# Kernel tuning notes

Measured on AMD Instinct MI355X. Metric: run time of the kernel, lower is better.

The kernel has to match this reference:

```python
import jax, jax.numpy as jnp
import numpy as np

EMBED_DIM = 1024
SCALE = float(np.sqrt(EMBED_DIM))


def setup_inputs() -> dict:
    key = jax.random.key(0)
    ks = jax.random.split(key, 4)
    B, S, D = 4, 2048, EMBED_DIM
    x = jax.random.normal(ks[0], (B, S, D), dtype=jnp.float32)
    # causal mask: 1 where attention allowed, 0 where blocked
    mask = jnp.tril(jnp.ones((S, S), dtype=jnp.int32))
    init = 1.0 / np.sqrt(D)
    Wq = jax.random.normal(ks[1], (D, D), dtype=jnp.float32) * init
    Wk = jax.random.normal(ks[2], (D, D), dtype=jnp.float32) * init
    Wv = jax.random.normal(ks[3], (D, D), dtype=jnp.float32) * init
    bq = jnp.zeros((D,), dtype=jnp.float32)
    bk = jnp.zeros((D,), dtype=jnp.float32)
    bv = jnp.zeros((D,), dtype=jnp.float32)
    return {"x": x, "mask": mask, "Wq": Wq, "bq": bq, "Wk": Wk, "bk": bk, "Wv": Wv, "bv": bv}


def reference(x, mask, Wq, bq, Wk, bk, Wv, bv):
    # Q, K, V projections (torch Linear: x @ W^T + b; here W stored as (D_in, D_out))
    q = x @ Wq + bq  # (B, S, D)
    k = x @ Wk + bk
    v = x @ Wv + bv
    # attention scores: Q K^T / sqrt(D)
    scores = jnp.einsum("bsd,btd->bst", q, k) / SCALE  # (B, S, S)
    scores = jnp.where(mask == 0, -jnp.inf, scores)
    attn = jax.nn.softmax(scores, axis=-1)
    # dropout disabled (inference / eval mode)
    out = jnp.einsum("bst,btd->bsd", attn, v)  # (B, S, D)
    return out
```

## Files before the change

### kernel.cpp

```cpp
#include <hip/hip_runtime.h>
#include <math.h>

#define DMODEL 1024
#define SEQ 2048
#define BATCH 4
#define SCALE_INV (1.0f/32.0f)

typedef unsigned short ushort_t;
typedef __attribute__((ext_vector_type(8))) short bf16x8;
typedef __attribute__((ext_vector_type(4))) float f32x4;

__device__ __forceinline__ ushort_t f2bf(float f) {
    unsigned int u = __float_as_uint(f);
    unsigned int rounding = 0x7FFFu + ((u >> 16) & 1u);
    return (ushort_t)((u + rounding) >> 16);
}

#define GLOAD16(SRC, DST) \
    __builtin_amdgcn_global_load_lds( \
        (const __attribute__((address_space(1))) void*)(SRC), \
        (__attribute__((address_space(3))) void*)(DST), 16, 0, 0)

__device__ __forceinline__ int xcd_swz(int bid, int nwg) {
    return (bid & 7) * (nwg >> 3) + (bid >> 3);
}

__device__ __forceinline__ void gemm_core_128(
    const ushort_t* __restrict__ A, int lda,
    const ushort_t* __restrict__ Bt, int ldb,
    int arow0, int brow0, int ksteps,
    ushort_t* As, ushort_t* Bs,
    f32x4 acc[4][4])
{
    const int tid = threadIdx.x;
    const int l   = tid & 63;
    const int w   = tid >> 6;
    const int wr  = w >> 1;
    const int wc  = w & 1;

    for (int s = 0; s < ksteps; ++s) {
        const int k0 = s * 32;
        #pragma unroll
        for (int i = 0; i < 2; ++i) {
            const int off = i * 4096 + w * 1024 + l * 16;
            const int row = off >> 6;
            const int ke  = (off & 63) >> 1;
            GLOAD16(A + (size_t)(arow0 + row) * lda + k0 + ke,
                    (char*)As + i * 4096 + w * 1024);
        }
        #pragma unroll
        for (int i = 0; i < 2; ++i) {
            const int off = i * 4096 + w * 1024 + l * 16;
            const int row = off >> 6;
            const int ke  = (off & 63) >> 1;
            GLOAD16(Bt + (size_t)(brow0 + row) * ldb + k0 + ke,
                    (char*)Bs + i * 4096 + w * 1024);
        }
        __syncthreads();

        bf16x8 a[4], b[4];
        #pragma unroll
        for (int m = 0; m < 4; ++m)
            a[m] = *(const bf16x8*)(As + (wr * 64 + m * 16 + (l & 15)) * 32 + (l >> 4) * 8);
        #pragma unroll
        for (int n = 0; n < 4; ++n)
            b[n] = *(const bf16x8*)(Bs + (wc * 64 + n * 16 + (l & 15)) * 32 + (l >> 4) * 8);
        #pragma unroll
        for (int m = 0; m < 4; ++m)
            #pragma unroll
            for (int n = 0; n < 4; ++n)
                acc[m][n] = __builtin_amdgcn_mfma_f32_16x16x32_bf16(a[m], b[n], acc[m][n], 0, 0, 0);
        __syncthreads();
    }
}

__global__ __launch_bounds__(256) void qkv_gemm_mfma(
    const ushort_t* __restrict__ x,
    const ushort_t* __restrict__ wt,
    const float* __restrict__ bq, const float* __restrict__ bk, const float* __restrict__ bv,
    ushort_t* __restrict__ q, ushort_t* __restrict__ k, ushort_t* __restrict__ vt)
{
    __shared__ __align__(16) ushort_t As[128 * 32];
    __shared__ __align__(16) ushort_t Bs[128 * 32];

    const int wg = xcd_swz(blockIdx.x, 8 * 64 * 3);
    const int z  = wg >> 9;
    const int r  = wg & 511;
    const int by = r >> 3;
    const int bx = r & 7;

    const ushort_t* Bt = wt + (size_t)z * DMODEL * DMODEL;
    const float* bias = (z == 0) ? bq : (z == 1) ? bk : bv;
    const float scale = (z == 0) ? SCALE_INV : 1.0f;

    const int arow0 = by * 128;
    const int brow0 = bx * 128;

    f32x4 acc[4][4];
    #pragma unroll
    for (int m = 0; m < 4; ++m)
        #pragma unroll
        for (int n = 0; n < 4; ++n)
            acc[m][n] = (f32x4)(0.f);

    gemm_core_128(x, DMODEL, Bt, DMODEL, arow0, brow0, DMODEL / 32, As, Bs, acc);

    const int l  = threadIdx.x & 63;
    const int w  = threadIdx.x >> 6;
    const int wr = w >> 1, wc = w & 1;

    if (z < 2) {
        ushort_t* out = (z == 0) ? q : k;
        #pragma unroll
        for (int n = 0; n < 4; ++n) {
            const int gcol = brow0 + wc * 64 + n * 16 + (l & 15);
            const float bb = bias[gcol];
            #pragma unroll
            for (int m = 0; m < 4; ++m) {
                #pragma unroll
                for (int j = 0; j < 4; ++j) {
                    const int grow = arow0 + wr * 64 + m * 16 + (l >> 4) * 4 + j;
                    out[(size_t)grow * DMODEL + gcol] = f2bf((acc[m][n][j] + bb) * scale);
                }
            }
        }
    } else {
        ushort_t* vtb = vt + (size_t)(arow0 >> 11) * DMODEL * SEQ;
        #pragma unroll
        for (int n = 0; n < 4; ++n) {
            const int gcol = brow0 + wc * 64 + n * 16 + (l & 15);
            const float bb = bias[gcol];
            #pragma unroll
            for (int m = 0; m < 4; ++m) {
                const int t0 = (arow0 & 2047) + wr * 64 + m * 16 + (l >> 4) * 4;
                ushort4 o;
                o.x = f2bf(acc[m][n][0] + bb);
                o.y = f2bf(acc[m][n][1] + bb);
                o.z = f2bf(acc[m][n][2] + bb);
                o.w = f2bf(acc[m][n][3] + bb);
                *(ushort4*)(vtb + (size_t)gcol * SEQ + t0) = o;
            }
        }
    }
}

__global__ __launch_bounds__(256) void qkt_exp_mfma(
    const ushort_t* __restrict__ q, const ushort_t* __restrict__ k,
    ushort_t* __restrict__ P, float* __restrict__ partials)
{
    const int wg = xcd_swz(blockIdx.x, 544);
    const int b  = wg / 136;
    const int i  = wg - b * 136;
    int st = (int)((sqrtf(8.f * (float)i + 1.f) - 1.f) * 0.5f);
    if (st * (st + 1) / 2 > i) st--;
    else if ((st + 1) * (st + 2) / 2 <= i) st++;
    const int tt = i - st * (st + 1) / 2;

    __shared__ __align__(16) ushort_t As[128 * 32];
    __shared__ __align__(16) ushort_t Bs[128 * 32];

    const ushort_t* A  = q + (size_t)b * SEQ * DMODEL;
    const ushort_t* Bt = k + (size_t)b * SEQ * DMODEL;

    f32x4 acc[4][4];
    #pragma unroll
    for (int m = 0; m < 4; ++m)
        #pragma unroll
        for (int n = 0; n < 4; ++n)
            acc[m][n] = (f32x4)(0.f);

    gemm_core_128(A, DMODEL, Bt, DMODEL, st * 128, tt * 128, DMODEL / 32, As, Bs, acc);

    const int l  = threadIdx.x & 63;
    const int w  = threadIdx.x >> 6;
    const int wr = w >> 1, wc = w & 1;
    ushort_t* pb = P + (size_t)b * SEQ * SEQ;
    float* part = partials + ((size_t)b * 32 + (size_t)(tt * 2 + wc)) * SEQ;
    const bool diag = (st == tt);

    #pragma unroll
    for (int m = 0; m < 4; ++m) {
        #pragma unroll
        for (int j = 0; j < 4; ++j) {
            const int grow = st * 128 + wr * 64 + m * 16 + (l >> 4) * 4 + j;
            float rs = 0.f;
            #pragma unroll
            for (int n = 0; n < 4; ++n) {
                const int gcol = tt * 128 + wc * 64 + n * 16 + (l & 15);
                float e = 0.f;
                if (!diag || gcol <= grow) e = __expf(acc[m][n][j]);
                rs += e;
                pb[(size_t)grow * SEQ + gcol] = f2bf(e);
            }
            rs += __shfl_xor(rs, 1);
            rs += __shfl_xor(rs, 2);
            rs += __shfl_xor(rs, 4);
            rs += __shfl_xor(rs, 8);
            if ((l & 15) == 0) part[grow] = rs;
        }
    }
}

__global__ __launch_bounds__(256) void combine_inv(
    const float* __restrict__ partials, float* __restrict__ inv)
{
    const int idx = blockIdx.x * 256 + threadIdx.x;
    const int b   = idx >> 11;
    const int row = idx & 2047;
    const int hmax = ((row >> 7) + 1) * 2;
    float s = 0.f;
    for (int h = 0; h < hmax; ++h)
        s += partials[((size_t)b * 32 + h) * SEQ + row];
    inv[idx] = 1.0f / s;
}

__global__ __launch_bounds__(256) void pv_gemm_mfma(
    const ushort_t* __restrict__ P, const ushort_t* __restrict__ vt,
    const float* __restrict__ inv, float* __restrict__ outp)
{
    const int wg = xcd_swz(blockIdx.x, 8 * 16 * BATCH);
    const int b  = wg >> 7;
    const int r  = wg & 127;
    const int st = r >> 3;
    const int dt = r & 7;

    __shared__ __align__(16) ushort_t As[128 * 32];
    __shared__ __align__(16) ushort_t Bs[128 * 32];

    const ushort_t* A  = P + (size_t)b * SEQ * SEQ;
    const ushort_t* Bt = vt + (size_t)b * DMODEL * SEQ;
    float* out = outp + (size_t)b * SEQ * DMODEL;
    const float* invb = inv + ((size_t)b << 11);

    f32x4 acc[4][4];
    #pragma unroll
    for (int m = 0; m < 4; ++m)
        #pragma unroll
        for (int n = 0; n < 4; ++n)
            acc[m][n] = (f32x4)(0.f);

    const int ksteps = (st + 1) * 4;
    gemm_core_128(A, SEQ, Bt, SEQ, st * 128, dt * 128, ksteps, As, Bs, acc);

    const int l  = threadIdx.x & 63;
    const int w  = threadIdx.x >> 6;
    const int wr = w >> 1, wc = w & 1;
    #pragma unroll
    for (int m = 0; m < 4; ++m) {
        #pragma unroll
        for (int j = 0; j < 4; ++j) {
            const int grow = st * 128 + wr * 64 + m * 16 + (l >> 4) * 4 + j;
            const float iv = invb[grow];
            #pragma unroll
            for (int n = 0; n < 4; ++n) {
                const int gcol = dt * 128 + wc * 64 + n * 16 + (l & 15);
                out[(size_t)grow * DMODEL + gcol] = acc[m][n][j] * iv;
            }
        }
    }
}

__global__ __launch_bounds__(256) void prep_kernel(
    const float* __restrict__ x, ushort_t* __restrict__ x_bf,
    const float* __restrict__ Wq, const float* __restrict__ Wk, const float* __restrict__ Wv,
    ushort_t* __restrict__ wt)
{
    __shared__ float tile[32][33];
    const int bid = blockIdx.x;
    const int tid = threadIdx.x;

    if (bid < 8192) {
        const int i = bid * 256 + tid;
        const float4 f = *(const float4*)(x + (size_t)i * 4);
        ushort4 o;
        o.x = f2bf(f.x); o.y = f2bf(f.y); o.z = f2bf(f.z); o.w = f2bf(f.w);
        *(ushort4*)(x_bf + (size_t)i * 4) = o;
    } else {
        const int id = bid - 8192;
        const int z  = id >> 10;
        const int t  = id & 1023;
        const int k0 = (t & 31) * 32;
        const int n0 = (t >> 5) * 32;
        const float* W = (z == 0) ? Wq : (z == 1) ? Wk : Wv;
        ushort_t* wtd = wt + (size_t)z * DMODEL * DMODEL;
        const int x_ = tid & 31, y = tid >> 5;
        #pragma unroll
        for (int i = 0; i < 4; ++i)
            tile[y + i * 8][x_] = W[(size_t)(k0 + y + i * 8) * DMODEL + n0 + x_];
        __syncthreads();
        #pragma unroll
        for (int i = 0; i < 4; ++i)
            wtd[(size_t)(n0 + y + i * 8) * DMODEL + k0 + x_] = f2bf(tile[x_][y + i * 8]);
    }
}

__global__ __launch_bounds__(1024) void qkv_gemm_f32(
    const float* __restrict__ x,
    const float* __restrict__ Wq, const float* __restrict__ bq,
    const float* __restrict__ Wk, const float* __restrict__ bk,
    const float* __restrict__ Wv, const float* __restrict__ bv,
    float* __restrict__ q, float* __restrict__ k, float* __restrict__ v)
{
    const float* W; const float* bias; float* out;
    const int z = blockIdx.z;
    if (z == 0)      { W = Wq; bias = bq; out = q; }
    else if (z == 1) { W = Wk; bias = bk; out = k; }
    else             { W = Wv; bias = bv; out = v; }

    __shared__ float As[32][33];
    __shared__ float Bs[32][33];
    const int tx = threadIdx.x, ty = threadIdx.y;
    const int row = blockIdx.y * 32 + ty;
    const int col = blockIdx.x * 32 + tx;

    float acc = 0.f;
    for (int k0 = 0; k0 < DMODEL; k0 += 32) {
        As[ty][tx] = x[(size_t)row * DMODEL + k0 + tx];
        Bs[ty][tx] = W[(size_t)(k0 + ty) * DMODEL + col];
        __syncthreads();
        #pragma unroll
        for (int kk = 0; kk < 32; ++kk)
            acc += As[ty][kk] * Bs[kk][tx];
        __syncthreads();
    }
    out[(size_t)row * DMODEL + col] = acc + bias[col];
}

__global__ __launch_bounds__(256) void attn_f32(
    const float* __restrict__ q, const float* __restrict__ k,
    const float* __restrict__ v, float* __restrict__ out)
{
    const int s = blockIdx.x, b = blockIdx.y, tid = threadIdx.x;
    __shared__ float qs[DMODEL];
    __shared__ float sc[SEQ];
    __shared__ float red[256];
    const float* qrow = q + ((size_t)b * SEQ + s) * DMODEL;
    for (int d = tid; d < DMODEL; d += 256) qs[d] = qrow[d];
    __syncthreads();
    const float* kb = k + (size_t)b * SEQ * DMODEL;
    const int nt = s + 1;
    float lmax = -INFINITY;
    for (int t = tid; t < nt; t += 256) {
        const float* krow = kb + (size_t)t * DMODEL;
        float acc = 0.f;
        for (int d = 0; d < DMODEL; d += 4) {
            const float4 kv = *(const float4*)(krow + d);
            acc += qs[d] * kv.x + qs[d+1] * kv.y + qs[d+2] * kv.z + qs[d+3] * kv.w;
        }
        acc *= SCALE_INV; sc[t] = acc; lmax = fmaxf(lmax, acc);
    }
    red[tid] = lmax; __syncthreads();
    for (int off = 128; off > 0; off >>= 1) { if (tid < off) red[tid] = fmaxf(red[tid], red[tid+off]); __syncthreads(); }
    const float mx = red[0]; __syncthreads();
    float lsum = 0.f;
    for (int t = tid; t < nt; t += 256) { const float e = expf(sc[t]-mx); sc[t]=e; lsum+=e; }
    red[tid] = lsum; __syncthreads();
    for (int off = 128; off > 0; off >>= 1) { if (tid < off) red[tid] += red[tid+off]; __syncthreads(); }
    const float inv = 1.0f / red[0]; __syncthreads();
    const float* vb = v + (size_t)b * SEQ * DMODEL;
    float a0=0,a1=0,a2=0,a3=0;
    for (int t = 0; t < nt; ++t) {
        const float p = sc[t];
        const float* vrow = vb + (size_t)t * DMODEL;
        a0 += p*vrow[tid]; a1 += p*vrow[tid+256]; a2 += p*vrow[tid+512]; a3 += p*vrow[tid+768];
    }
    float* orow = out + ((size_t)b * SEQ + s) * DMODEL;
    orow[tid]=a0*inv; orow[tid+256]=a1*inv; orow[tid+512]=a2*inv; orow[tid+768]=a3*inv;
}

extern "C" void kernel_launch(void* const* d_in, const int* in_sizes, int n_in,
                              void* d_out, int out_size, void* d_ws, size_t ws_size,
                              hipStream_t stream)
{
    const float* x  = (const float*)d_in[0];
    const float* Wq = (const float*)d_in[2];
    const float* bq = (const float*)d_in[3];
    const float* Wk = (const float*)d_in[4];
    const float* bk = (const float*)d_in[5];
    const float* Wv = (const float*)d_in[6];
    const float* bv = (const float*)d_in[7];
    float* out = (float*)d_out;

    const size_t SZ_XBF  = (size_t)BATCH * SEQ * DMODEL * 2;
    const size_t SZ_WT   = 3 * (size_t)DMODEL * DMODEL * 2;
    const size_t SZ_QKV  = (size_t)BATCH * SEQ * DMODEL * 2;
    const size_t SZ_P    = (size_t)BATCH * SEQ * SEQ * 2;
    const size_t SZ_PART = (size_t)BATCH * 32 * SEQ * 4;
    const size_t SZ_INV  = (size_t)BATCH * SEQ * 4;
    const size_t NEED = SZ_XBF + SZ_WT + 3 * SZ_QKV + SZ_P + SZ_PART + SZ_INV;

    if (ws_size >= NEED) {
        char* p = (char*)d_ws;
        ushort_t* x_bf = (ushort_t*)p;              p += SZ_XBF;
        ushort_t* wt   = (ushort_t*)p;              p += SZ_WT;
        ushort_t* q_bf = (ushort_t*)p;              p += SZ_QKV;
        ushort_t* k_bf = (ushort_t*)p;              p += SZ_QKV;
        ushort_t* vt   = (ushort_t*)p;              p += SZ_QKV;
        ushort_t* Pb   = (ushort_t*)p;              p += SZ_P;
        float*    part = (float*)p;                 p += SZ_PART;
        float*    inv  = (float*)p;

        hipLaunchKernelGGL(prep_kernel, dim3(8192 + 3072), dim3(256), 0, stream,
                           x, x_bf, Wq, Wk, Wv, wt);
        hipLaunchKernelGGL(qkv_gemm_mfma, dim3(8 * 64 * 3), dim3(256), 0, stream,
                           x_bf, wt, bq, bk, bv, q_bf, k_bf, vt);
        hipLaunchKernelGGL(qkt_exp_mfma, dim3(544), dim3(256), 0, stream,
                           q_bf, k_bf, Pb, part);
        hipLaunchKernelGGL(combine_inv, dim3(32), dim3(256), 0, stream, part, inv);
        hipLaunchKernelGGL(pv_gemm_mfma, dim3(8 * 16 * BATCH), dim3(256), 0, stream,
                           Pb, vt, inv, out);
    } else {
        const size_t elems = (size_t)BATCH * SEQ * DMODEL;
        float* q = (float*)d_ws;
        float* k = q + elems;
        float* v = k + elems;
        hipLaunchKernelGGL(qkv_gemm_f32, dim3(DMODEL / 32, BATCH * SEQ / 32, 3), dim3(32, 32), 0, stream,
                           x, Wq, bq, Wk, bk, Wv, bv, q, k, v);
        hipLaunchKernelGGL(attn_f32, dim3(SEQ, BATCH), dim3(256), 0, stream, q, k, v, out);
    }
}
```

Baseline: 178.4 us.

## Double-buffer LDS tiles in GEMM core and fold row-sum combine into PV kernel

The shared GEMM core now uses two LDS buffer pairs, so the global-to-LDS load for the next K step is issued before computing on the current tile, with one barrier per step instead of two. Separately, the combine_inv kernel is removed. Each PV workgroup now sums the partial row sums itself into LDS, which saves a launch and a global round trip. The costs are double the LDS per block, which may lower occupancy, and redundant partial-sum reads across the 8 dt tiles.

After: 171.4 us, median of 4. -3.9%, faster.

```diff
diff --git a/kernel.cpp b/kernel.cpp
--- a/kernel.cpp
+++ b/kernel.cpp
@@ -25,11 +25,45 @@
     return (bid & 7) * (nwg >> 3) + (bid >> 3);
 }
 
+#define STAGE_TILE(ASP, BSP, K0) do { \
+    _Pragma("unroll") \
+    for (int i_ = 0; i_ < 2; ++i_) { \
+        const int off_ = i_ * 4096 + w * 1024 + l * 16; \
+        const int row_ = off_ >> 6; \
+        const int ke_  = (off_ & 63) >> 1; \
+        GLOAD16(A + (size_t)(arow0 + row_) * lda + (K0) + ke_, \
+                (char*)(ASP) + i_ * 4096 + w * 1024); \
+    } \
+    _Pragma("unroll") \
+    for (int i_ = 0; i_ < 2; ++i_) { \
+        const int off_ = i_ * 4096 + w * 1024 + l * 16; \
+        const int row_ = off_ >> 6; \
+        const int ke_  = (off_ & 63) >> 1; \
+        GLOAD16(Bt + (size_t)(brow0 + row_) * ldb + (K0) + ke_, \
+                (char*)(BSP) + i_ * 4096 + w * 1024); \
+    } \
+} while (0)
+
+#define COMPUTE_TILE(ASP, BSP) do { \
+    bf16x8 a_[4], b_[4]; \
+    _Pragma("unroll") \
+    for (int m_ = 0; m_ < 4; ++m_) \
+        a_[m_] = *(const bf16x8*)((ASP) + (wr * 64 + m_ * 16 + (l & 15)) * 32 + (l >> 4) * 8); \
+    _Pragma("unroll") \
+    for (int n_ = 0; n_ < 4; ++n_) \
+        b_[n_] = *(const bf16x8*)((BSP) + (wc * 64 + n_ * 16 + (l & 15)) * 32 + (l >> 4) * 8); \
+    _Pragma("unroll") \
+    for (int m_ = 0; m_ < 4; ++m_) \
+        _Pragma("unroll") \
+        for (int n_ = 0; n_ < 4; ++n_) \
+            acc[m_][n_] = __builtin_amdgcn_mfma_f32_16x16x32_bf16(a_[m_], b_[n_], acc[m_][n_], 0, 0, 0); \
+} while (0)
+
 __device__ __forceinline__ void gemm_core_128(
     const ushort_t* __restrict__ A, int lda,
     const ushort_t* __restrict__ Bt, int ldb,
     int arow0, int brow0, int ksteps,
-    ushort_t* As, ushort_t* Bs,
+    ushort_t* As0, ushort_t* Bs0, ushort_t* As1, ushort_t* Bs1,
     f32x4 acc[4][4])
 {
     const int tid = threadIdx.x;
@@ -38,39 +72,20 @@
     const int wr  = w >> 1;
     const int wc  = w & 1;
 
-    for (int s = 0; s < ksteps; ++s) {
-        const int k0 = s * 32;
-        #pragma unroll
-        for (int i = 0; i < 2; ++i) {
-            const int off = i * 4096 + w * 1024 + l * 16;
-            const int row = off >> 6;
-            const int ke  = (off & 63) >> 1;
-            GLOAD16(A + (size_t)(arow0 + row) * lda + k0 + ke,
-                    (char*)As + i * 4096 + w * 1024);
-        }
-        #pragma unroll
-        for (int i = 0; i < 2; ++i) {
-            const int off = i * 4096 + w * 1024 + l * 16;
-            const int row = off >> 6;
-            const int ke  = (off & 63) >> 1;
-            GLOAD16(Bt + (size_t)(brow0 + row) * ldb + k0 + ke,
-                    (char*)Bs + i * 4096 + w * 1024);
-        }
+    STAGE_TILE(As0, Bs0, 0);
+    __syncthreads();
+
+    int s = 0;
+    while (true) {
+        if (s + 1 < ksteps) STAGE_TILE(As1, Bs1, (s + 1) * 32);
+        COMPUTE_TILE(As0, Bs0);
         __syncthreads();
-
-        bf16x8 a[4], b[4];
-        #pragma unroll
-        for (int m = 0; m < 4; ++m)
-            a[m] = *(const bf16x8*)(As + (wr * 64 + m * 16 + (l & 15)) * 32 + (l >> 4) * 8);
-        #pragma unroll
-        for (int n = 0; n < 4; ++n)
-            b[n] = *(const bf16x8*)(Bs + (wc * 64 + n * 16 + (l & 15)) * 32 + (l >> 4) * 8);
-        #pragma unroll
-        for (int m = 0; m < 4; ++m)
-            #pragma unroll
-            for (int n = 0; n < 4; ++n)
-                acc[m][n] = __builtin_amdgcn_mfma_f32_16x16x32_bf16(a[m], b[n], acc[m][n], 0, 0, 0);
+        if (++s >= ksteps) break;
+
+        if (s + 1 < ksteps) STAGE_TILE(As0, Bs0, (s + 1) * 32);
+        COMPUTE_TILE(As1, Bs1);
         __syncthreads();
+        if (++s >= ksteps) break;
     }
 }
 
@@ -80,8 +95,10 @@
     const float* __restrict__ bq, const float* __restrict__ bk, const float* __restrict__ bv,
     ushort_t* __restrict__ q, ushort_t* __restrict__ k, ushort_t* __restrict__ vt)
 {
-    __shared__ __align__(16) ushort_t As[128 * 32];
-    __shared__ __align__(16) ushort_t Bs[128 * 32];
+    __shared__ __align__(16) ushort_t As0[128 * 32];
+    __shared__ __align__(16) ushort_t Bs0[128 * 32];
+    __shared__ __align__(16) ushort_t As1[128 * 32];
+    __shared__ __align__(16) ushort_t Bs1[128 * 32];
 
     const int wg = xcd_swz(blockIdx.x, 8 * 64 * 3);
     const int z  = wg >> 9;
@@ -103,7 +120,8 @@
         for (int n = 0; n < 4; ++n)
             acc[m][n] = (f32x4)(0.f);
 
-    gemm_core_128(x, DMODEL, Bt, DMODEL, arow0, brow0, DMODEL / 32, As, Bs, acc);
+    gemm_core_128(x, DMODEL, Bt, DMODEL, arow0, brow0, DMODEL / 32,
+                  As0, Bs0, As1, Bs1, acc);
 
     const int l  = threadIdx.x & 63;
     const int w  = threadIdx.x >> 6;
@@ -156,8 +174,10 @@
     else if ((st + 1) * (st + 2) / 2 <= i) st++;
     const int tt = i - st * (st + 1) / 2;
 
-    __shared__ __align__(16) ushort_t As[128 * 32];
-    __shared__ __align__(16) ushort_t Bs[128 * 32];
+    __shared__ __align__(16) ushort_t As0[128 * 32];
+    __shared__ __align__(16) ushort_t Bs0[128 * 32];
+    __shared__ __align__(16) ushort_t As1[128 * 32];
+    __shared__ __align__(16) ushort_t Bs1[128 * 32];
 
     const ushort_t* A  = q + (size_t)b * SEQ * DMODEL;
     const ushort_t* Bt = k + (size_t)b * SEQ * DMODEL;
@@ -169,7 +189,8 @@
         for (int n = 0; n < 4; ++n)
             acc[m][n] = (f32x4)(0.f);
 
-    gemm_core_128(A, DMODEL, Bt, DMODEL, st * 128, tt * 128, DMODEL / 32, As, Bs, acc);
+    gemm_core_128(A, DMODEL, Bt, DMODEL, st * 128, tt * 128, DMODEL / 32,
+                  As0, Bs0, As1, Bs1, acc);
 
     const int l  = threadIdx.x & 63;
     const int w  = threadIdx.x >> 6;
@@ -201,22 +222,9 @@
     }
 }
 
-__global__ __launch_bounds__(256) void combine_inv(
-    const float* __restrict__ partials, float* __restrict__ inv)
-{
-    const int idx = blockIdx.x * 256 + threadIdx.x;
-    const int b   = idx >> 11;
-    const int row = idx & 2047;
-    const int hmax = ((row >> 7) + 1) * 2;
-    float s = 0.f;
-    for (int h = 0; h < hmax; ++h)
-        s += partials[((size_t)b * 32 + h) * SEQ + row];
-    inv[idx] = 1.0f / s;
-}
-
 __global__ __launch_bounds__(256) void pv_gemm_mfma(
     const ushort_t* __restrict__ P, const ushort_t* __restrict__ vt,
-    const float* __restrict__ inv, float* __restrict__ outp)
+    const float* __restrict__ partials, float* __restrict__ outp)
 {
     const int wg = xcd_swz(blockIdx.x, 8 * 16 * BATCH);
     const int b  = wg >> 7;
@@ -224,13 +232,25 @@
     const int st = r >> 3;
     const int dt = r & 7;
 
-    __shared__ __align__(16) ushort_t As[128 * 32];
-    __shared__ __align__(16) ushort_t Bs[128 * 32];
+    __shared__ __align__(16) ushort_t As0[128 * 32];
+    __shared__ __align__(16) ushort_t Bs0[128 * 32];
+    __shared__ __align__(16) ushort_t As1[128 * 32];
+    __shared__ __align__(16) ushort_t Bs1[128 * 32];
+    __shared__ float inv_lds[128];
+
+    const int tid = threadIdx.x;
+    if (tid < 128) {
+        const int grow = st * 128 + tid;
+        const int hmax = (st + 1) * 2;
+        float ssum = 0.f;
+        for (int h = 0; h < hmax; ++h)
+            ssum += partials[((size_t)b * 32 + h) * SEQ + grow];
+        inv_lds[tid] = 1.0f / ssum;
+    }
 
     const ushort_t* A  = P + (size_t)b * SEQ * SEQ;
     const ushort_t* Bt = vt + (size_t)b * DMODEL * SEQ;
     float* out = outp + (size_t)b * SEQ * DMODEL;
-    const float* invb = inv + ((size_t)b << 11);
 
     f32x4 acc[4][4];
     #pragma unroll
@@ -240,7 +260,8 @@
             acc[m][n] = (f32x4)(0.f);
 
     const int ksteps = (st + 1) * 4;
-    gemm_core_128(A, SEQ, Bt, SEQ, st * 128, dt * 128, ksteps, As, Bs, acc);
+    gemm_core_128(A, SEQ, Bt, SEQ, st * 128, dt * 128, ksteps,
+                  As0, Bs0, As1, Bs1, acc);
 
     const int l  = threadIdx.x & 63;
     const int w  = threadIdx.x >> 6;
@@ -249,8 +270,9 @@
     for (int m = 0; m < 4; ++m) {
         #pragma unroll
         for (int j = 0; j < 4; ++j) {
-            const int grow = st * 128 + wr * 64 + m * 16 + (l >> 4) * 4 + j;
-            const float iv = invb[grow];
+            const int lrow = wr * 64 + m * 16 + (l >> 4) * 4 + j;
+            const int grow = st * 128 + lrow;
+            const float iv = inv_lds[lrow];
             #pragma unroll
             for (int n = 0; n < 4; ++n) {
                 const int gcol = dt * 128 + wc * 64 + n * 16 + (l & 15);
@@ -386,8 +408,7 @@
     const size_t SZ_QKV  = (size_t)BATCH * SEQ * DMODEL * 2;
     const size_t SZ_P    = (size_t)BATCH * SEQ * SEQ * 2;
     const size_t SZ_PART = (size_t)BATCH * 32 * SEQ * 4;
-    const size_t SZ_INV  = (size_t)BATCH * SEQ * 4;
-    const size_t NEED = SZ_XBF + SZ_WT + 3 * SZ_QKV + SZ_P + SZ_PART + SZ_INV;
+    const size_t NEED = SZ_XBF + SZ_WT + 3 * SZ_QKV + SZ_P + SZ_PART;
 
     if (ws_size >= NEED) {
         char* p = (char*)d_ws;
@@ -397,8 +418,7 @@
         ushort_t* k_bf = (ushort_t*)p;              p += SZ_QKV;
         ushort_t* vt   = (ushort_t*)p;              p += SZ_QKV;
         ushort_t* Pb   = (ushort_t*)p;              p += SZ_P;
-        float*    part = (float*)p;                 p += SZ_PART;
-        float*    inv  = (float*)p;
+        float*    part = (float*)p;
 
         hipLaunchKernelGGL(prep_kernel, dim3(8192 + 3072), dim3(256), 0, stream,
                            x, x_bf, Wq, Wk, Wv, wt);
@@ -406,9 +426,8 @@
                            x_bf, wt, bq, bk, bv, q_bf, k_bf, vt);
         hipLaunchKernelGGL(qkt_exp_mfma, dim3(544), dim3(256), 0, stream,
                            q_bf, k_bf, Pb, part);
-        hipLaunchKernelGGL(combine_inv, dim3(32), dim3(256), 0, stream, part, inv);
         hipLaunchKernelGGL(pv_gemm_mfma, dim3(8 * 16 * BATCH), dim3(256), 0, stream,
-                           Pb, vt, inv, out);
+                           Pb, vt, part, out);
     } else {
         const size_t elems = (size_t)BATCH * SEQ * DMODEL;
         float* q = (float*)d_ws;
```
